# Kernel tuning notes

Measured on AMD Instinct MI355X. Metric: run time of the kernel, lower is better.

Reference implementation:

```python
import jax, jax.numpy as jnp
import numpy as np

N_NODES = 50000
HIDDEN = 128
N_EDGES = 600000
DROPOUT_RATE = 0.25


def setup_inputs() -> dict:
    key = jax.random.key(0)
    k_x, k_e, k_w1, k_w2 = jax.random.split(key, 4)
    x = jax.random.normal(k_x, (N_NODES, HIDDEN), dtype=jnp.float32)
    edge_index = jax.random.randint(k_e, (2, N_EDGES), 0, N_NODES, dtype=jnp.int64)
    # Linear layers: torch Linear default init ~ U(-1/sqrt(fan_in), 1/sqrt(fan_in))
    s = 1.0 / np.sqrt(HIDDEN)
    W1 = jax.random.uniform(k_w1, (HIDDEN, HIDDEN), jnp.float32, -s, s)
    b1 = jnp.zeros((HIDDEN,), jnp.float32)
    W2 = jax.random.uniform(k_w2, (HIDDEN, HIDDEN), jnp.float32, -s, s)
    b2 = jnp.zeros((HIDDEN,), jnp.float32)
    return {"x": x, "edge_index": edge_index, "W1": W1, "b1": b1, "W2": W2, "b2": b2}


def reference(x, edge_index, W1, b1, W2, b2):
    # Feature-dim dropout mask (bernoulli over hidden dim, broadcast over nodes).
    mask_key = jax.random.key(42)
    mask = jax.random.bernoulli(mask_key, 1.0 - DROPOUT_RATE, (x.shape[1],)).astype(x.dtype)
    xd = x * mask[None, :]  # [N, D]

    # GINConv aggregation: sum of source-node features at destination nodes.
    src, dst = edge_index[0], edge_index[1]
    agg = jax.ops.segment_sum(xd[src], dst, num_segments=x.shape[0])  # [N, D]

    # (1 + eps) * x + agg, eps = 0 (GINConv default)
    h = xd + agg

    # 2-layer MLP: Linear -> ReLU -> Linear
    h = jax.nn.relu(h @ W1 + b1)
    out = h @ W2 + b2
    return out
```

## Files before the change

### kernel.cpp

```cpp
#include <hip/hip_runtime.h>

#define N_NODES 50000
#define HIDDEN  128
#define N_EDGES 600000
#define BR      32
#define NB      ((N_NODES + 255) / 256)
#define NTILES  ((N_NODES + BR - 1) / BR)
#define E_PAD_MAX (N_EDGES + 3 * N_NODES)

typedef __attribute__((ext_vector_type(8))) short short8v;
typedef __attribute__((ext_vector_type(4))) float f32x4;

__device__ __forceinline__ unsigned rotl32(unsigned v, int r) {
  return (v << r) | (v >> (32 - r));
}

__device__ __forceinline__ void threefry2x32(unsigned x0, unsigned x1,
                                             unsigned& o0, unsigned& o1) {
  const unsigned ks0 = 0u, ks1 = 42u;
  const unsigned ks2 = ks0 ^ ks1 ^ 0x1BD11BDAu;
  const unsigned ks[3] = {ks0, ks1, ks2};
  const int rot[2][4] = {{13, 15, 26, 6}, {17, 29, 16, 24}};
  x0 += ks0; x1 += ks1;
#pragma unroll
  for (int i = 0; i < 5; ++i) {
#pragma unroll
    for (int j = 0; j < 4; ++j) {
      x0 += x1;
      x1 = rotl32(x1, rot[i & 1][j]);
      x1 ^= x0;
    }
    x0 += ks[(i + 1) % 3];
    x1 += ks[(i + 2) % 3] + (unsigned)(i + 1);
  }
  o0 = x0; o1 = x1;
}

__device__ __forceinline__ float col_mask(int c) {
  unsigned o0, o1;
  threefry2x32(0u, (unsigned)c, o0, o1);
  unsigned bits = o0 ^ o1;
  float u = __uint_as_float((bits >> 9) | 0x3f800000u) - 1.0f;
  return (u < 0.75f) ? 1.0f : 0.0f;
}

__device__ __forceinline__ unsigned short f2bf(float f) {
  unsigned u = __float_as_uint(f);
  u += 0x7fffu + ((u >> 16) & 1u);
  return (unsigned short)(u >> 16);
}

__device__ __forceinline__ float bflo(unsigned u) {
  return __uint_as_float(u << 16);
}
__device__ __forceinline__ float bfhi(unsigned u) {
  return __uint_as_float(u & 0xffff0000u);
}

__device__ __forceinline__ float rlane(float v, int l) {
  return __int_as_float(__builtin_amdgcn_readlane(__float_as_int(v), l));
}

__global__ __launch_bounds__(256) void prep_kernel(
    const float* __restrict__ x, const float* __restrict__ W1,
    const float* __restrict__ W2, const int* __restrict__ ei,
    unsigned short* __restrict__ xb, unsigned short* __restrict__ Wt1,
    unsigned short* __restrict__ Wt2, int* __restrict__ deg) {
  __shared__ float msk[HIDDEN];
  if (threadIdx.x < HIDDEN) msk[threadIdx.x] = col_mask(threadIdx.x);
  __syncthreads();

  const int gid = blockIdx.x * 256 + threadIdx.x;
  const int e0 = gid * 8;
  if (e0 < N_NODES * HIDDEN) {
    const int c0 = e0 & (HIDDEN - 1);
    const float4 v0 = *reinterpret_cast<const float4*>(x + e0);
    const float4 v1 = *reinterpret_cast<const float4*>(x + e0 + 4);
    unsigned short h[8];
    h[0] = f2bf(v0.x * msk[c0 + 0]);
    h[1] = f2bf(v0.y * msk[c0 + 1]);
    h[2] = f2bf(v0.z * msk[c0 + 2]);
    h[3] = f2bf(v0.w * msk[c0 + 3]);
    h[4] = f2bf(v1.x * msk[c0 + 4]);
    h[5] = f2bf(v1.y * msk[c0 + 5]);
    h[6] = f2bf(v1.z * msk[c0 + 6]);
    h[7] = f2bf(v1.w * msk[c0 + 7]);
    *reinterpret_cast<uint4*>(xb + e0) = *reinterpret_cast<uint4*>(h);
  }
  if (gid < N_EDGES) atomicAdd(deg + ei[N_EDGES + gid], 1);
  if (gid < HIDDEN * HIDDEN / 4) {
#pragma unroll
    for (int i = 0; i < 4; ++i) {
      int t = gid * 4 + i;
      int col = t >> 7, k = t & 127;
      Wt1[t] = f2bf(W1[k * HIDDEN + col]);
      Wt2[t] = f2bf(W2[k * HIDDEN + col]);
    }
  }
  if (gid < 16) {
    uint4 z; z.x = 0; z.y = 0; z.z = 0; z.w = 0;
    *reinterpret_cast<uint4*>(xb + (size_t)N_NODES * HIDDEN + gid * 8) = z;
  }
}

__global__ __launch_bounds__(256) void scanA_kernel(const int* __restrict__ deg,
                                                    int* __restrict__ bsum) {
  int idx = blockIdx.x * 256 + threadIdx.x;
  int v = (idx < N_NODES) ? ((deg[idx] + 3) & ~3) : 0;
#pragma unroll
  for (int off = 32; off; off >>= 1) v += __shfl_down(v, off, 64);
  __shared__ int ws4[4];
  if ((threadIdx.x & 63) == 0) ws4[threadIdx.x >> 6] = v;
  __syncthreads();
  if (threadIdx.x == 0) bsum[blockIdx.x] = ws4[0] + ws4[1] + ws4[2] + ws4[3];
}

__global__ __launch_bounds__(256) void scanB_kernel(const int* __restrict__ bsum,
                                                    int* __restrict__ bpre,
                                                    int* __restrict__ offs) {
  __shared__ int s[256];
  const int t = threadIdx.x;
  int v = (t < NB) ? bsum[t] : 0;
  s[t] = v;
  __syncthreads();
  int acc = v;
  for (int off = 1; off < 256; off <<= 1) {
    int add = (t >= off) ? s[t - off] : 0;
    __syncthreads();
    acc += add;
    s[t] = acc;
    __syncthreads();
  }
  if (t < NB) bpre[t] = acc - v;
  if (t == 0) offs[N_NODES] = s[255];
}

__global__ __launch_bounds__(256) void scanC_kernel(
    const int* __restrict__ deg, const int* __restrict__ bpre,
    int* __restrict__ offs, int* __restrict__ pos,
    unsigned short* __restrict__ csr) {
  __shared__ int s[256];
  const int t = threadIdx.x;
  const int idx = blockIdx.x * 256 + t;
  int d = (idx < N_NODES) ? deg[idx] : 0;
  int v = (d + 3) & ~3;
  s[t] = v;
  __syncthreads();
  int acc = v;
  for (int off = 1; off < 256; off <<= 1) {
    int add = (t >= off) ? s[t - off] : 0;
    __syncthreads();
    acc += add;
    s[t] = acc;
    __syncthreads();
  }
  if (idx < N_NODES) {
    int o = bpre[blockIdx.x] + acc - v;
    offs[idx] = o;
    pos[idx] = o;
    for (int w = o + d; w < o + v; ++w)
      csr[w] = (unsigned short)N_NODES;
  }
}

__global__ __launch_bounds__(256) void fill_kernel(const int* __restrict__ ei,
                                                   int* __restrict__ pos,
                                                   unsigned short* __restrict__ csr) {
  int e = blockIdx.x * blockDim.x + threadIdx.x;
  if (e >= N_EDGES) return;
  int src = ei[e];
  int dst = ei[N_EDGES + e];
  int p = atomicAdd(pos + dst, 1);
  csr[p] = (unsigned short)src;
}

__global__ __launch_bounds__(256) void fused_xb_kernel(
    const int* __restrict__ offs, const unsigned short* __restrict__ csr,
    const unsigned short* __restrict__ xb,
    const unsigned short* __restrict__ Wt1,
    const unsigned short* __restrict__ Wt2, const float* __restrict__ b1,
    const float* __restrict__ b2, float* __restrict__ out) {
  __shared__ unsigned short H1[BR * HIDDEN];
  __shared__ unsigned short H2[BR * HIDDEN];

  const int tid = threadIdx.x;
  const int lane = tid & 63;
  const int wave = tid >> 6;
  const int half = lane >> 5;
  const int hl = lane & 31;
  const int base = blockIdx.x * BR;

#pragma unroll 1
  for (int i = 0; i < 4; ++i) {
    const int row = wave * 8 + 2 * i + half;
    const int node = base + row;
    const bool valid = node < N_NODES;
    const int na = valid ? node : 0;
    int s = offs[na];
    int e = offs[na + 1];
    s = valid ? s : 0;
    e = valid ? e : 0;
    const int on = valid ? node : N_NODES;
    const uint2 ov =
        *reinterpret_cast<const uint2*>(xb + (size_t)on * HIDDEN + hl * 4);
    float a0 = bflo(ov.x), a1 = bfhi(ov.x);
    float a2 = bflo(ov.y), a3 = bfhi(ov.y);

    const int it = (e - s) >> 2;
    const int m = max(__builtin_amdgcn_readlane(it, 0),
                      __builtin_amdgcn_readlane(it, 32));
    int j = s;
    for (int t = 0; t < m; ++t) {
      const bool v4 = j < e;
      const int jc = v4 ? j : 0;
      const int i0 = v4 ? (int)csr[jc + 0] : N_NODES;
      const int i1 = v4 ? (int)csr[jc + 1] : N_NODES;
      const int i2 = v4 ? (int)csr[jc + 2] : N_NODES;
      const int i3 = v4 ? (int)csr[jc + 3] : N_NODES;
      const uint2 u0 =
          *reinterpret_cast<const uint2*>(xb + (size_t)i0 * HIDDEN + hl * 4);
      const uint2 u1 =
          *reinterpret_cast<const uint2*>(xb + (size_t)i1 * HIDDEN + hl * 4);
      const uint2 u2 =
          *reinterpret_cast<const uint2*>(xb + (size_t)i2 * HIDDEN + hl * 4);
      const uint2 u3 =
          *reinterpret_cast<const uint2*>(xb + (size_t)i3 * HIDDEN + hl * 4);
      a0 += bflo(u0.x) + bflo(u1.x) + bflo(u2.x) + bflo(u3.x);
      a1 += bfhi(u0.x) + bfhi(u1.x) + bfhi(u2.x) + bfhi(u3.x);
      a2 += bflo(u0.y) + bflo(u1.y) + bflo(u2.y) + bflo(u3.y);
      a3 += bfhi(u0.y) + bfhi(u1.y) + bfhi(u2.y) + bfhi(u3.y);
      j += 4;
    }
    unsigned p0 = (unsigned)f2bf(a0) | ((unsigned)f2bf(a1) << 16);
    unsigned p1 = (unsigned)f2bf(a2) | ((unsigned)f2bf(a3) << 16);
    const int byte = (row * 256 + hl * 8) ^ ((row & 7) << 4);
    uint2 pw; pw.x = p0; pw.y = p1;
    *reinterpret_cast<uint2*>(reinterpret_cast<char*>(H1) + byte) = pw;
  }
  __syncthreads();

  const int colbase = wave * 32;
  float bias1[2], bias2[2];
#pragma unroll
  for (int c = 0; c < 2; ++c) {
    bias1[c] = b1[colbase + c * 16 + (lane & 15)];
    bias2[c] = b2[colbase + c * 16 + (lane & 15)];
  }

  f32x4 acc[2][2] = {};
#pragma unroll
  for (int kt = 0; kt < 4; ++kt) {
    short8v a[2], b[2];
#pragma unroll
    for (int r = 0; r < 2; ++r) {
      int row = r * 16 + (lane & 15);
      int byte = (row * 256 + kt * 64 + (lane >> 4) * 16) ^ ((row & 7) << 4);
      a[r] = *reinterpret_cast<const short8v*>(
          reinterpret_cast<const char*>(H1) + byte);
    }
#pragma unroll
    for (int c = 0; c < 2; ++c) {
      int col = colbase + c * 16 + (lane & 15);
      b[c] = *reinterpret_cast<const short8v*>(
          reinterpret_cast<const char*>(Wt1) + col * 256 + kt * 64 +
          (lane >> 4) * 16);
    }
#pragma unroll
    for (int r = 0; r < 2; ++r)
#pragma unroll
      for (int c = 0; c < 2; ++c)
        acc[r][c] = __builtin_amdgcn_mfma_f32_16x16x32_bf16(a[r], b[c],
                                                            acc[r][c], 0, 0, 0);
  }
#pragma unroll
  for (int r = 0; r < 2; ++r)
#pragma unroll
    for (int c = 0; c < 2; ++c)
#pragma unroll
      for (int q = 0; q < 4; ++q) {
        int row = r * 16 + (lane >> 4) * 4 + q;
        int col = colbase + c * 16 + (lane & 15);
        float v = fmaxf(acc[r][c][q] + bias1[c], 0.f);
        int byte = (row * 256 + col * 2) ^ ((row & 7) << 4);
        *reinterpret_cast<unsigned short*>(reinterpret_cast<char*>(H2) + byte) =
            f2bf(v);
      }
  __syncthreads();

  f32x4 acc2[2][2] = {};
#pragma unroll
  for (int kt = 0; kt < 4; ++kt) {
    short8v a[2], b[2];
#pragma unroll
    for (int r = 0; r < 2; ++r) {
      int row = r * 16 + (lane & 15);
      int byte = (row * 256 + kt * 64 + (lane >> 4) * 16) ^ ((row & 7) << 4);
      a[r] = *reinterpret_cast<const short8v*>(
          reinterpret_cast<const char*>(H2) + byte);
    }
#pragma unroll
    for (int c = 0; c < 2; ++c) {
      int col = colbase + c * 16 + (lane & 15);
      b[c] = *reinterpret_cast<const short8v*>(
          reinterpret_cast<const char*>(Wt2) + col * 256 + kt * 64 +
          (lane >> 4) * 16);
    }
#pragma unroll
    for (int r = 0; r < 2; ++r)
#pragma unroll
      for (int c = 0; c < 2; ++c)
        acc2[r][c] = __builtin_amdgcn_mfma_f32_16x16x32_bf16(
            a[r], b[c], acc2[r][c], 0, 0, 0);
  }
#pragma unroll
  for (int r = 0; r < 2; ++r)
#pragma unroll
    for (int c = 0; c < 2; ++c)
#pragma unroll
      for (int q = 0; q < 4; ++q) {
        int row = base + r * 16 + (lane >> 4) * 4 + q;
        if (row < N_NODES) {
          int col = colbase + c * 16 + (lane & 15);
          out[(size_t)row * HIDDEN + col] = acc2[r][c][q] + bias2[c];
        }
      }
}

__global__ __launch_bounds__(256) void scatter_kernel(
    const int* __restrict__ ei, const float* __restrict__ x,
    float* __restrict__ agg) {
  long long gid = (long long)blockIdx.x * blockDim.x + threadIdx.x;
  int e = (int)(gid >> 5);
  if (e >= N_EDGES) return;
  int sub = ((int)gid & 31) * 4;
  int src = ei[e];
  int dst = ei[N_EDGES + e];
  const float4 v = *reinterpret_cast<const float4*>(x + src * HIDDEN + sub);
  float* p = agg + dst * HIDDEN + sub;
  atomicAdd(p + 0, v.x);
  atomicAdd(p + 1, v.y);
  atomicAdd(p + 2, v.z);
  atomicAdd(p + 3, v.w);
}

__global__ __launch_bounds__(512) void mlp_kernel(
    const float* __restrict__ x, float* __restrict__ io,
    const float* __restrict__ W1, const float* __restrict__ b1,
    const float* __restrict__ W2, const float* __restrict__ b2) {
  __shared__ float W1s[HIDDEN * HIDDEN];
  __shared__ float W2s[HIDDEN * HIDDEN];

  const int tid = threadIdx.x;
#pragma unroll
  for (int i = 0; i < 8; ++i) {
    int idx = (i * 512 + tid) * 4;
    *reinterpret_cast<float4*>(W1s + idx) =
        *reinterpret_cast<const float4*>(W1 + idx);
    *reinterpret_cast<float4*>(W2s + idx) =
        *reinterpret_cast<const float4*>(W2 + idx);
  }

  const int lane = tid & 63;
  const int wave = tid >> 6;
  const int c0 = 2 * lane, c1 = 2 * lane + 1;

  const float m0 = col_mask(c0);
  const float m1 = col_mask(c1);
  const float bb1x = b1[c0], bb1y = b1[c1];
  const float bb2x = b2[c0], bb2y = b2[c1];

  __syncthreads();

  const int gwave = blockIdx.x * 8 + wave;
  const int nwaves = gridDim.x * 8;

  for (int pr = gwave; pr < N_NODES / 2; pr += nwaves) {
    const int baseA = (2 * pr) * HIDDEN;
    const int baseB = baseA + HIDDEN;

    float2 xA = *reinterpret_cast<const float2*>(x + baseA + c0);
    float2 gA = *reinterpret_cast<const float2*>(io + baseA + c0);
    float2 xB = *reinterpret_cast<const float2*>(x + baseB + c0);
    float2 gB = *reinterpret_cast<const float2*>(io + baseB + c0);

    float hA0 = m0 * (xA.x + gA.x), hA1 = m1 * (xA.y + gA.y);
    float hB0 = m0 * (xB.x + gB.x), hB1 = m1 * (xB.y + gB.y);

    float aA0 = bb1x, aA1 = bb1y, aB0 = bb1x, aB1 = bb1y;
#pragma unroll
    for (int k = 0; k < HIDDEN; ++k) {
      const int sl = k >> 1;
      float hkA = (k & 1) ? rlane(hA1, sl) : rlane(hA0, sl);
      float hkB = (k & 1) ? rlane(hB1, sl) : rlane(hB0, sl);
      float2 w = *reinterpret_cast<const float2*>(W1s + k * HIDDEN + c0);
      aA0 = fmaf(hkA, w.x, aA0);
      aA1 = fmaf(hkA, w.y, aA1);
      aB0 = fmaf(hkB, w.x, aB0);
      aB1 = fmaf(hkB, w.y, aB1);
    }
    aA0 = fmaxf(aA0, 0.0f); aA1 = fmaxf(aA1, 0.0f);
    aB0 = fmaxf(aB0, 0.0f); aB1 = fmaxf(aB1, 0.0f);

    float oA0 = bb2x, oA1 = bb2y, oB0 = bb2x, oB1 = bb2y;
#pragma unroll
    for (int k = 0; k < HIDDEN; ++k) {
      const int sl = k >> 1;
      float hkA = (k & 1) ? rlane(aA1, sl) : rlane(aA0, sl);
      float hkB = (k & 1) ? rlane(aB1, sl) : rlane(aB0, sl);
      float2 w = *reinterpret_cast<const float2*>(W2s + k * HIDDEN + c0);
      oA0 = fmaf(hkA, w.x, oA0);
      oA1 = fmaf(hkA, w.y, oA1);
      oB0 = fmaf(hkB, w.x, oB0);
      oB1 = fmaf(hkB, w.y, oB1);
    }

    *reinterpret_cast<float2*>(io + baseA + c0) = make_float2(oA0, oA1);
    *reinterpret_cast<float2*>(io + baseB + c0) = make_float2(oB0, oB1);
  }
}

extern "C" void kernel_launch(void* const* d_in, const int* in_sizes, int n_in,
                              void* d_out, int out_size, void* d_ws,
                              size_t ws_size, hipStream_t stream) {
  (void)in_sizes; (void)n_in; (void)out_size;
  const float* x  = (const float*)d_in[0];
  const int*   ei = (const int*)d_in[1];
  const float* W1 = (const float*)d_in[2];
  const float* b1 = (const float*)d_in[3];
  const float* W2 = (const float*)d_in[4];
  const float* b2 = (const float*)d_in[5];
  float* out = (float*)d_out;

  const size_t int_bytes = (size_t)(N_NODES + (N_NODES + 1) + N_NODES + 2 * NB) * 4;
  const size_t int_pad   = (int_bytes + 15) & ~(size_t)15;
  const size_t csr_bytes = (size_t)E_PAD_MAX * 2;
  const size_t wt_bytes  = 2 * (size_t)HIDDEN * HIDDEN * 2;
  const size_t xb_bytes  = (size_t)(N_NODES + 1) * HIDDEN * 2;
  const size_t need = int_pad + csr_bytes + wt_bytes + xb_bytes;

  if (ws_size >= need) {
    char* wsb = (char*)d_ws;
    int* deg  = (int*)wsb;
    int* offs = deg + N_NODES;
    int* pos  = offs + N_NODES + 1;
    int* bsum = pos + N_NODES;
    int* bpre = bsum + NB;
    unsigned short* csr = (unsigned short*)(wsb + int_pad);
    unsigned short* Wt1 = (unsigned short*)(wsb + int_pad + csr_bytes);
    unsigned short* Wt2 = Wt1 + HIDDEN * HIDDEN;
    unsigned short* xb  = Wt2 + HIDDEN * HIDDEN;

    hipMemsetAsync(deg, 0, (size_t)N_NODES * 4, stream);
    const int nprep = (N_NODES * HIDDEN / 8 + 255) / 256;
    prep_kernel<<<nprep, 256, 0, stream>>>(x, W1, W2, ei, xb, Wt1, Wt2, deg);
    scanA_kernel<<<NB, 256, 0, stream>>>(deg, bsum);
    scanB_kernel<<<1, 256, 0, stream>>>(bsum, bpre, offs);
    scanC_kernel<<<NB, 256, 0, stream>>>(deg, bpre, offs, pos, csr);
    fill_kernel<<<(N_EDGES + 255) / 256, 256, 0, stream>>>(ei, pos, csr);
    fused_xb_kernel<<<NTILES, 256, 0, stream>>>(offs, csr, xb, Wt1, Wt2, b1,
                                                b2, out);
  } else {
    hipMemsetAsync(out, 0, (size_t)N_NODES * HIDDEN * sizeof(float), stream);
    const long long total = (long long)N_EDGES * 32;
    scatter_kernel<<<(int)((total + 255) / 256), 256, 0, stream>>>(ei, x, out);
    mlp_kernel<<<256, 512, 0, stream>>>(x, out, W1, b1, W2, b2);
  }
}
```

Before: 125.6 us.

## Stage block CSR indices in LDS and gather 4 rows per wave with 16B loads

The fused gather-MLP kernel now copies the block's row offsets and CSR neighbour indices into shared memory before gathering. It also remaps lanes so each wave handles four rows at a time with 16 lanes per row and 16-byte loads, replacing 32 lanes with 8-byte loads. Four packed indices are read with one 8-byte load and prefetched one iteration ahead. The aim is fewer scattered 2-byte global index loads, less per-row loop divergence and wider memory transactions, at the cost of more LDS and an extra staging pass with a barrier.

```diff
diff --git a/kernel.cpp b/kernel.cpp
--- a/kernel.cpp
+++ b/kernel.cpp
@@ -7,6 +7,7 @@
 #define NB      ((N_NODES + 255) / 256)
 #define NTILES  ((N_NODES + BR - 1) / BR)
 #define E_PAD_MAX (N_EDGES + 3 * N_NODES)
+#define SCSR_CAP 4096
 
 typedef __attribute__((ext_vector_type(8))) short short8v;
 typedef __attribute__((ext_vector_type(4))) float f32x4;
@@ -174,6 +175,67 @@
   csr[p] = (unsigned short)src;
 }
 
+template <bool LDSIDX>
+__device__ __forceinline__ void gather2(
+    int base, int wave, int q, int ql, int cs,
+    const unsigned short* __restrict__ csr, const unsigned short* scsr,
+    const int* loffs, const unsigned short* __restrict__ xb,
+    unsigned short* H1) {
+#pragma unroll
+  for (int i = 0; i < 2; ++i) {
+    const int row = wave * 8 + i * 4 + q;
+    const int node = base + row;
+    const bool valid = node < N_NODES;
+    const int s = valid ? loffs[row] : 0;
+    const int e = valid ? loffs[row + 1] : 0;
+    const int on = valid ? node : N_NODES;
+    const uint4 ov =
+        *reinterpret_cast<const uint4*>(xb + (size_t)on * HIDDEN + ql * 8);
+    float a0 = bflo(ov.x), a1 = bfhi(ov.x);
+    float a2 = bflo(ov.y), a3 = bfhi(ov.y);
+    float a4 = bflo(ov.z), a5 = bfhi(ov.z);
+    float a6 = bflo(ov.w), a7 = bfhi(ov.w);
+
+    uint2 pk; pk.x = 0; pk.y = 0;
+    if (s < e) {
+      pk = LDSIDX ? *reinterpret_cast<const uint2*>(scsr + (s - cs))
+                  : *reinterpret_cast<const uint2*>(csr + s);
+    }
+    for (int j = s; j < e; j += 4) {
+      const unsigned px = pk.x, py = pk.y;
+      if (j + 4 < e) {
+        pk = LDSIDX ? *reinterpret_cast<const uint2*>(scsr + (j + 4 - cs))
+                    : *reinterpret_cast<const uint2*>(csr + j + 4);
+      }
+      const int i0 = (int)(px & 0xffffu), i1 = (int)(px >> 16);
+      const int i2 = (int)(py & 0xffffu), i3 = (int)(py >> 16);
+      const uint4 u0 =
+          *reinterpret_cast<const uint4*>(xb + (size_t)i0 * HIDDEN + ql * 8);
+      const uint4 u1 =
+          *reinterpret_cast<const uint4*>(xb + (size_t)i1 * HIDDEN + ql * 8);
+      const uint4 u2 =
+          *reinterpret_cast<const uint4*>(xb + (size_t)i2 * HIDDEN + ql * 8);
+      const uint4 u3 =
+          *reinterpret_cast<const uint4*>(xb + (size_t)i3 * HIDDEN + ql * 8);
+      a0 += bflo(u0.x) + bflo(u1.x) + bflo(u2.x) + bflo(u3.x);
+      a1 += bfhi(u0.x) + bfhi(u1.x) + bfhi(u2.x) + bfhi(u3.x);
+      a2 += bflo(u0.y) + bflo(u1.y) + bflo(u2.y) + bflo(u3.y);
+      a3 += bfhi(u0.y) + bfhi(u1.y) + bfhi(u2.y) + bfhi(u3.y);
+      a4 += bflo(u0.z) + bflo(u1.z) + bflo(u2.z) + bflo(u3.z);
+      a5 += bfhi(u0.z) + bfhi(u1.z) + bfhi(u2.z) + bfhi(u3.z);
+      a6 += bflo(u0.w) + bflo(u1.w) + bflo(u2.w) + bflo(u3.w);
+      a7 += bfhi(u0.w) + bfhi(u1.w) + bfhi(u2.w) + bfhi(u3.w);
+    }
+    uint4 pw;
+    pw.x = (unsigned)f2bf(a0) | ((unsigned)f2bf(a1) << 16);
+    pw.y = (unsigned)f2bf(a2) | ((unsigned)f2bf(a3) << 16);
+    pw.z = (unsigned)f2bf(a4) | ((unsigned)f2bf(a5) << 16);
+    pw.w = (unsigned)f2bf(a6) | ((unsigned)f2bf(a7) << 16);
+    const int byte = (row * 256 + ql * 16) ^ ((row & 7) << 4);
+    *reinterpret_cast<uint4*>(reinterpret_cast<char*>(H1) + byte) = pw;
+  }
+}
+
 __global__ __launch_bounds__(256) void fused_xb_kernel(
     const int* __restrict__ offs, const unsigned short* __restrict__ csr,
     const unsigned short* __restrict__ xb,
@@ -182,61 +244,36 @@
     const float* __restrict__ b2, float* __restrict__ out) {
   __shared__ unsigned short H1[BR * HIDDEN];
   __shared__ unsigned short H2[BR * HIDDEN];
+  __shared__ unsigned short scsr[SCSR_CAP];
+  __shared__ int loffs[BR + 1];
 
   const int tid = threadIdx.x;
   const int lane = tid & 63;
   const int wave = tid >> 6;
-  const int half = lane >> 5;
-  const int hl = lane & 31;
   const int base = blockIdx.x * BR;
 
-#pragma unroll 1
-  for (int i = 0; i < 4; ++i) {
-    const int row = wave * 8 + 2 * i + half;
-    const int node = base + row;
-    const bool valid = node < N_NODES;
-    const int na = valid ? node : 0;
-    int s = offs[na];
-    int e = offs[na + 1];
-    s = valid ? s : 0;
-    e = valid ? e : 0;
-    const int on = valid ? node : N_NODES;
-    const uint2 ov =
-        *reinterpret_cast<const uint2*>(xb + (size_t)on * HIDDEN + hl * 4);
-    float a0 = bflo(ov.x), a1 = bfhi(ov.x);
-    float a2 = bflo(ov.y), a3 = bfhi(ov.y);
-
-    const int it = (e - s) >> 2;
-    const int m = max(__builtin_amdgcn_readlane(it, 0),
-                      __builtin_amdgcn_readlane(it, 32));
-    int j = s;
-    for (int t = 0; t < m; ++t) {
-      const bool v4 = j < e;
-      const int jc = v4 ? j : 0;
-      const int i0 = v4 ? (int)csr[jc + 0] : N_NODES;
-      const int i1 = v4 ? (int)csr[jc + 1] : N_NODES;
-      const int i2 = v4 ? (int)csr[jc + 2] : N_NODES;
-      const int i3 = v4 ? (int)csr[jc + 3] : N_NODES;
-      const uint2 u0 =
-          *reinterpret_cast<const uint2*>(xb + (size_t)i0 * HIDDEN + hl * 4);
-      const uint2 u1 =
-          *reinterpret_cast<const uint2*>(xb + (size_t)i1 * HIDDEN + hl * 4);
-      const uint2 u2 =
-          *reinterpret_cast<const uint2*>(xb + (size_t)i2 * HIDDEN + hl * 4);
-      const uint2 u3 =
-          *reinterpret_cast<const uint2*>(xb + (size_t)i3 * HIDDEN + hl * 4);
-      a0 += bflo(u0.x) + bflo(u1.x) + bflo(u2.x) + bflo(u3.x);
-      a1 += bfhi(u0.x) + bfhi(u1.x) + bfhi(u2.x) + bfhi(u3.x);
-      a2 += bflo(u0.y) + bflo(u1.y) + bflo(u2.y) + bflo(u3.y);
-      a3 += bfhi(u0.y) + bfhi(u1.y) + bfhi(u2.y) + bfhi(u3.y);
-      j += 4;
-    }
-    unsigned p0 = (unsigned)f2bf(a0) | ((unsigned)f2bf(a1) << 16);
-    unsigned p1 = (unsigned)f2bf(a2) | ((unsigned)f2bf(a3) << 16);
-    const int byte = (row * 256 + hl * 8) ^ ((row & 7) << 4);
-    uint2 pw; pw.x = p0; pw.y = p1;
-    *reinterpret_cast<uint2*>(reinterpret_cast<char*>(H1) + byte) = pw;
-  }
+  if (tid < BR + 1) {
+    int idx = base + tid;
+    loffs[tid] = offs[idx > N_NODES ? N_NODES : idx];
+  }
+  __syncthreads();
+  const int cs = loffs[0];
+  const int count = loffs[BR] - cs;
+  const bool stage = (count <= SCSR_CAP);
+  if (stage) {
+    const unsigned* src = reinterpret_cast<const unsigned*>(csr + cs);
+    unsigned* dst = reinterpret_cast<unsigned*>(scsr);
+    for (int k = tid; k < (count >> 1); k += 256) dst[k] = src[k];
+  }
+  __syncthreads();
+
+  const int q = lane >> 4;
+  const int ql = lane & 15;
+
+  if (stage)
+    gather2<true>(base, wave, q, ql, cs, csr, scsr, loffs, xb, H1);
+  else
+    gather2<false>(base, wave, q, ql, cs, csr, scsr, loffs, xb, H1);
   __syncthreads();
 
   const int colbase = wave * 32;
@@ -277,10 +314,10 @@
 #pragma unroll
     for (int c = 0; c < 2; ++c)
 #pragma unroll
-      for (int q = 0; q < 4; ++q) {
-        int row = r * 16 + (lane >> 4) * 4 + q;
+      for (int q2 = 0; q2 < 4; ++q2) {
+        int row = r * 16 + (lane >> 4) * 4 + q2;
         int col = colbase + c * 16 + (lane & 15);
-        float v = fmaxf(acc[r][c][q] + bias1[c], 0.f);
+        float v = fmaxf(acc[r][c][q2] + bias1[c], 0.f);
         int byte = (row * 256 + col * 2) ^ ((row & 7) << 4);
         *reinterpret_cast<unsigned short*>(reinterpret_cast<char*>(H2) + byte) =
             f2bf(v);
@@ -317,11 +354,11 @@
 #pragma unroll
     for (int c = 0; c < 2; ++c)
 #pragma unroll
-      for (int q = 0; q < 4; ++q) {
-        int row = base + r * 16 + (lane >> 4) * 4 + q;
+      for (int q2 = 0; q2 < 4; ++q2) {
+        int row = base + r * 16 + (lane >> 4) * 4 + q2;
         if (row < N_NODES) {
           int col = colbase + c * 16 + (lane & 15);
-          out[(size_t)row * HIDDEN + col] = acc2[r][c][q] + bias2[c];
+          out[(size_t)row * HIDDEN + col] = acc2[r][c][q2] + bias2[c];
         }
       }
 }
```

Measured after the change: 117.8 us. 1.07x faster.
